# Performance work log

Measured on AMD Instinct MI355X. Metric: run time of the kernel, lower is better.

Reference implementation:

```python
import jax, jax.numpy as jnp
import numpy as np

N = 50000
E = 1600000
IN_DIM = 64
EMB_DIM = 64
DENSE = 128
HEADS = 2
GATD = 64
SLOPE = 0.2


def gat_conv(x, src, dst, W, al, ar, b):
    # DGL GATConv: x [N, Fin], W [Fin, H*D], al/ar/b [H, D]
    n = x.shape[0]
    H, D = al.shape
    z = (x @ W).reshape(n, H, D)                      # [N,H,D]
    el = jnp.sum(z * al, axis=-1)                     # [N,H]
    er = jnp.sum(z * ar, axis=-1)                     # [N,H]
    e = jax.nn.leaky_relu(el[src] + er[dst], SLOPE)   # [E,H]
    # edge softmax grouped by destination node
    m = jax.ops.segment_max(e, dst, num_segments=n)   # [N,H]
    ex = jnp.exp(e - m[dst])                          # [E,H]
    s = jax.ops.segment_sum(ex, dst, num_segments=n)  # [N,H]
    alpha = ex / s[dst]                               # [E,H]
    out = jax.ops.segment_sum(alpha[:, :, None] * z[src], dst, num_segments=n)
    return out + b                                    # [N,H,D]


def setup_inputs() -> dict:
    key = jax.random.key(0)
    ks = jax.random.split(key, 20)
    g = lambda k, sh: jax.random.normal(k, sh, dtype=jnp.float32) * 0.05
    inp = {
        "feat": jax.random.normal(ks[0], (N, IN_DIM), dtype=jnp.float32),
        "node_ids": jax.random.randint(ks[1], (N,), 0, N, dtype=jnp.int32),
        "src": jax.random.randint(ks[2], (E,), 0, N, dtype=jnp.int32),
        "dst": jax.random.randint(ks[3], (E,), 0, N, dtype=jnp.int32),
        "emb": g(ks[4], (N, EMB_DIM)),
        "dense_w": g(ks[5], (IN_DIM + EMB_DIM, DENSE)),
        "dense_b": jnp.zeros((DENSE,), jnp.float32),
        "g1_w": g(ks[6], (DENSE, HEADS * GATD)),
        "g1_al": g(ks[7], (HEADS, GATD)),
        "g1_ar": g(ks[8], (HEADS, GATD)),
        "g1_b": jnp.zeros((HEADS, GATD), jnp.float32),
        "g2_w": g(ks[9], (HEADS * GATD, HEADS * GATD)),
        "g2_al": g(ks[10], (HEADS, GATD)),
        "g2_ar": g(ks[11], (HEADS, GATD)),
        "g2_b": jnp.zeros((HEADS, GATD), jnp.float32),
        "out_w": g(ks[12], (HEADS * GATD, 1)),
        "out_al": g(ks[13], (1, 1)),
        "out_ar": g(ks[14], (1, 1)),
        "out_b": jnp.zeros((1, 1), jnp.float32),
    }
    return inp


def reference(feat, node_ids, src, dst, emb, dense_w, dense_b,
              g1_w, g1_al, g1_ar, g1_b, g2_w, g2_al, g2_ar, g2_b,
              out_w, out_al, out_ar, out_b):
    # embedding concat + initial dense + ReLU
    h = jnp.concatenate([emb[node_ids], feat], axis=-1)   # [N, 128]
    h = jax.nn.relu(h @ dense_w + dense_b)                # [N, 128]
    # GAT layer 1: ReLU then concat heads (reshape N, H*D)
    h = jax.nn.relu(gat_conv(h, src, dst, g1_w, g1_al, g1_ar, g1_b))
    h = h.reshape(h.shape[0], -1)                         # [N, H*D]
    # GAT layer 2
    h = jax.nn.relu(gat_conv(h, src, dst, g2_w, g2_al, g2_ar, g2_b))
    h = h.reshape(h.shape[0], -1)
    # output GAT layer, 1 head, squeeze head dim
    h = gat_conv(h, src, dst, out_w, out_al, out_ar, out_b)  # [N,1,1]
    return h[:, 0, :]                                        # [N,1]
```

## Files before the change

kernel.cpp:

```cpp
#include <hip/hip_runtime.h>
#include <cfloat>
#include <cmath>


#define CBG 256
#define CAPC 12288
#define TILE 8192
#define BIMG 10240

typedef __attribute__((ext_vector_type(8))) short short8v;
typedef __attribute__((ext_vector_type(4))) float f32x4;

__device__ __forceinline__ float lrelu(float x) { return x > 0.f ? x : 0.2f * x; }

__device__ __forceinline__ uint32_t bf16_rne(float f) {
  uint32_t u = __float_as_uint(f);
  return (u + 0x7fffu + ((u >> 16) & 1u)) >> 16;
}
__device__ __forceinline__ uint32_t pack_hilo(float v) {
  uint32_t h = bf16_rne(v);
  float r = v - __uint_as_float(h << 16);
  return (h << 16) | bf16_rne(r);
}

__global__ __launch_bounds__(256) void bucketA_kernel(
    const int* __restrict__ src, const int* __restrict__ dst,
    int* __restrict__ scount, uint32_t* __restrict__ tmp, int e, int ncb) {
  __shared__ int cnt[256];
  __shared__ int lscan[256];
  __shared__ int gbase[256];
  __shared__ uint32_t image[TILE];
  const int t = threadIdx.x;
  const int e0 = blockIdx.x * TILE;
  const int ne = min(TILE, e - e0);

  for (int i = t; i < 256; i += 256) cnt[i] = 0;
  __syncthreads();
  for (int i = t; i < ne; i += 256) atomicAdd(&cnt[dst[e0 + i] >> 8], 1);
  __syncthreads();
  if (t < 64) {
    int carry = 0;
    for (int base = 0; base < ncb; base += 64) {
      int idx = base + t;
      int c = (idx < ncb) ? cnt[idx] : 0;
      int v = c;
#pragma unroll
      for (int off = 1; off < 64; off <<= 1) {
        int u = __shfl_up(v, off, 64);
        if (t >= off) v += u;
      }
      if (idx < ncb) lscan[idx] = carry + v - c;
      carry += __shfl(v, 63, 64);
    }
  }
  __syncthreads();
  for (int b = t; b < ncb; b += 256)
    gbase[b] = (cnt[b] > 0) ? atomicAdd(&scount[b], cnt[b]) : 0;
  __syncthreads();
  for (int b = t; b < ncb; b += 256) cnt[b] = 0;
  __syncthreads();
  for (int i = t; i < ne; i += 256) {
    int d = dst[e0 + i], s = src[e0 + i];
    int b = d >> 8;
    int r = atomicAdd(&cnt[b], 1);
    image[lscan[b] + r] =
        (uint32_t)s | ((uint32_t)(d & 255) << 16) | ((uint32_t)b << 24);
  }
  __syncthreads();
  for (int j = t; j < ne; j += 256) {
    uint32_t w = image[j];
    int b = w >> 24;
    int pos = gbase[b] + (j - lscan[b]);
    if (pos < CAPC) tmp[(size_t)b * CAPC + pos] = w & 0xFFFFFFu;
  }
}

__global__ __launch_bounds__(64) void scanS_kernel(const int* __restrict__ scount,
                                                   int* __restrict__ sbase,
                                                   int* __restrict__ row_start,
                                                   int ncb, int n, int e) {
  const int lane = threadIdx.x;
  int carry = 0;
  for (int base = 0; base < ncb; base += 64) {
    int idx = base + lane;
    int c = (idx < ncb) ? scount[idx] : 0;
    int v = c;
#pragma unroll
    for (int off = 1; off < 64; off <<= 1) {
      int u = __shfl_up(v, off, 64);
      if (lane >= off) v += u;
    }
    if (idx < ncb) sbase[idx] = carry + v - c;
    carry += __shfl(v, 63, 64);
  }
  if (lane == 0) row_start[n] = e;
}

__global__ __launch_bounds__(256) void bucketB_kernel(
    const uint32_t* __restrict__ tmp, const int* __restrict__ scount,
    const int* __restrict__ sbase, int* __restrict__ row_start,
    int* __restrict__ csr_src, int n, int ncb) {
  __shared__ int cnt[256];
  __shared__ int cur[256];
  __shared__ int wsum[4];
  __shared__ uint32_t image[BIMG];
  const int b = blockIdx.x, t = threadIdx.x, lane = t & 63, wid = t >> 6;
  const int total = min(scount[b], CAPC);
  const int base = sbase[b];
  const uint32_t* strm = tmp + (size_t)b * CAPC;

  cnt[t] = 0;
  __syncthreads();
  for (int i = t; i < total; i += 256) atomicAdd(&cnt[(strm[i] >> 16) & 255], 1);
  __syncthreads();
  int c = cnt[t], v = c;
#pragma unroll
  for (int off = 1; off < 64; off <<= 1) {
    int u = __shfl_up(v, off, 64);
    if (lane >= off) v += u;
  }
  if (lane == 63) wsum[wid] = v;
  __syncthreads();
  if (t == 0) {
    int acc = 0;
#pragma unroll
    for (int w = 0; w < 4; w++) { int x = wsum[w]; wsum[w] = acc; acc += x; }
  }
  __syncthreads();
  int ex = wsum[wid] + v - c;
  cur[t] = ex;
  int d = b * CBG + t;
  if (d < n) row_start[d] = base + ex;
  __syncthreads();
  for (int i = t; i < total; i += 256) {
    uint32_t w = strm[i];
    int dl = (w >> 16) & 255;
    int pos = atomicAdd(&cur[dl], 1);
    if (pos < BIMG) image[pos] = w & 0xFFFFu;
    else csr_src[base + pos] = (int)(w & 0xFFFFu);
  }
  __syncthreads();
  const int lim = total < BIMG ? total : BIMG;
  for (int j = t; j < lim; j += 256) csr_src[base + j] = (int)image[j];
}

__global__ void hist_kernel(const int* __restrict__ dst, int* __restrict__ cnt, int e) {
  for (int i = blockIdx.x * blockDim.x + threadIdx.x; i < e; i += gridDim.x * blockDim.x)
    atomicAdd(&cnt[dst[i]], 1);
}
__global__ void scatter_kernel(const int* __restrict__ src, const int* __restrict__ dst,
                               const int* __restrict__ row_start, int* __restrict__ cursor,
                               int* __restrict__ csr_src, int e) {
  for (int i = blockIdx.x * blockDim.x + threadIdx.x; i < e; i += gridDim.x * blockDim.x) {
    int d = dst[i];
    int pos = atomicAdd(&cursor[d], 1);
    csr_src[row_start[d] + pos] = src[i];
  }
}
__global__ __launch_bounds__(1024) void scan1_kernel(const int* __restrict__ cnt,
                                                     int* __restrict__ row_start,
                                                     int* __restrict__ bsum, int n) {
  __shared__ int wsum[16];
  const int t = threadIdx.x, lane = t & 63, wid = t >> 6;
  int i = blockIdx.x * 1024 + t;
  int c = (i < n) ? cnt[i] : 0;
  int v = c;
#pragma unroll
  for (int off = 1; off < 64; off <<= 1) {
    int u = __shfl_up(v, off, 64);
    if (lane >= off) v += u;
  }
  if (lane == 63) wsum[wid] = v;
  __syncthreads();
  if (t == 0) {
    int acc = 0;
#pragma unroll
    for (int w = 0; w < 16; w++) { int x = wsum[w]; wsum[w] = acc; acc += x; }
    bsum[blockIdx.x] = acc;
  }
  __syncthreads();
  if (i < n) row_start[i] = wsum[wid] + v - c;
}
__global__ __launch_bounds__(64) void scan2_kernel(int* __restrict__ bsum, int nb) {
  const int lane = threadIdx.x;
  int carry = 0;
  for (int base = 0; base < nb; base += 64) {
    int idx = base + lane;
    int c = (idx < nb) ? bsum[idx] : 0;
    int v = c;
#pragma unroll
    for (int off = 1; off < 64; off <<= 1) {
      int u = __shfl_up(v, off, 64);
      if (lane >= off) v += u;
    }
    if (idx < nb) bsum[idx] = carry + v - c;
    carry += __shfl(v, 63, 64);
  }
}
__global__ void scan3_kernel(int* __restrict__ row_start, const int* __restrict__ bsum,
                             int n, int e) {
  int i = blockIdx.x * blockDim.x + threadIdx.x;
  if (i < n) row_start[i] += bsum[i >> 10];
  if (i == 0) row_start[n] = e;
}

__global__ __launch_bounds__(256) void wswz_kernel(const float* __restrict__ W,
                                                   short* __restrict__ Whi,
                                                   short* __restrict__ Wlo) {
  int fid = blockIdx.x * 256 + threadIdx.x;
  if (fid >= 2048) return;
  int lane = fid & 63;
  int cq = fid >> 6;
  int q = cq >> 3, c = cq & 7;
  int col = c * 16 + (lane & 15);
  int k0 = q * 32 + (lane >> 4) * 8;
  short hi[8], lo[8];
#pragma unroll
  for (int j = 0; j < 8; j++) {
    float v = W[(k0 + j) * 128 + col];
    uint32_t h = bf16_rne(v);
    float r = v - __uint_as_float(h << 16);
    hi[j] = (short)h;
    lo[j] = (short)bf16_rne(r);
  }
#pragma unroll
  for (int j = 0; j < 8; j++) {
    Whi[fid * 8 + j] = hi[j];
    Wlo[fid * 8 + j] = lo[j];
  }
}

template <int MODE>
__global__ __launch_bounds__(256) void mfmm_kernel(
    const uint32_t* __restrict__ Xp, const short* __restrict__ Whi,
    const short* __restrict__ Wlo, const float* __restrict__ bias,
    uint32_t* __restrict__ Hp, uint32_t* __restrict__ zp,
    float2* __restrict__ el2, float2* __restrict__ er2,
    const float* __restrict__ al, const float* __restrict__ ar, int n,
    const float* __restrict__ emb, const int* __restrict__ ids,
    const float* __restrict__ feat) {
  __shared__ short Ahi[64 * 136];
  __shared__ short Alo[64 * 136];
  const int t = threadIdx.x;
  const int nb = blockIdx.x * 64;

  for (int idx = t; idx < 64 * 64; idx += 256) {
    int nl = idx >> 6, k2 = (idx & 63) << 1;
    int node = nb + nl;
    uint32_t whi = 0, wlo = 0;
    if (node < n) {
      if (MODE == 1) {
        uint2 w = *(const uint2*)&Xp[(size_t)node * 128 + k2];
        whi = (w.x >> 16) | (w.y & 0xffff0000u);
        wlo = (w.x & 0xffffu) | (w.y << 16);
      } else {
        float2 v;
        if (k2 < 64) v = *(const float2*)&emb[(size_t)ids[node] * 64 + k2];
        else         v = *(const float2*)&feat[(size_t)node * 64 + (k2 - 64)];
        uint32_t h0 = bf16_rne(v.x), h1 = bf16_rne(v.y);
        float r0 = v.x - __uint_as_float(h0 << 16);
        float r1 = v.y - __uint_as_float(h1 << 16);
        whi = h0 | (h1 << 16);
        wlo = bf16_rne(r0) | (bf16_rne(r1) << 16);
      }
    }
    *(uint32_t*)&Ahi[nl * 136 + k2] = whi;
    *(uint32_t*)&Alo[nl * 136 + k2] = wlo;
  }
  __syncthreads();

  const int lane = t & 63, wv = t >> 6;
  const int r16 = lane & 15, g = lane >> 4;
  const int arow = (wv * 16 + r16) * 136;

  f32x4 acc[8];
#pragma unroll
  for (int c = 0; c < 8; c++) acc[c] = (f32x4){0.f, 0.f, 0.f, 0.f};

#pragma unroll
  for (int q = 0; q < 4; q++) {
    int ka = q * 32 + g * 8;
    short8v ahi = *(const short8v*)&Ahi[arow + ka];
    short8v alo = *(const short8v*)&Alo[arow + ka];
#pragma unroll
    for (int c = 0; c < 8; c++) {
      short8v bhi = *(const short8v*)&Whi[(((q * 8 + c) * 64) + lane) * 8];
      short8v blo = *(const short8v*)&Wlo[(((q * 8 + c) * 64) + lane) * 8];
      acc[c] = __builtin_amdgcn_mfma_f32_16x16x32_bf16(ahi, bhi, acc[c], 0, 0, 0);
      acc[c] = __builtin_amdgcn_mfma_f32_16x16x32_bf16(ahi, blo, acc[c], 0, 0, 0);
      acc[c] = __builtin_amdgcn_mfma_f32_16x16x32_bf16(alo, bhi, acc[c], 0, 0, 0);
    }
  }

  const int node_base = nb + wv * 16;
  if (MODE == 0) {
#pragma unroll
    for (int c = 0; c < 8; c++) {
      int col = c * 16 + r16;
      float bv = bias[col];
#pragma unroll
      for (int r = 0; r < 4; r++) {
        int node = node_base + g * 4 + r;
        if (node < n) {
          float v = fmaxf(acc[c][r] + bv, 0.f);
          Hp[(size_t)node * 128 + col] = pack_hilo(v);
        }
      }
    }
  } else {
    float p0l[4] = {0, 0, 0, 0}, p1l[4] = {0, 0, 0, 0};
    float p0r[4] = {0, 0, 0, 0}, p1r[4] = {0, 0, 0, 0};
#pragma unroll
    for (int c = 0; c < 8; c++) {
      int col = c * 16 + r16;
      float av = al[col], rv = ar[col];
#pragma unroll
      for (int r = 0; r < 4; r++) {
        if (c < 4) { p0l[r] = fmaf(acc[c][r], av, p0l[r]); p0r[r] = fmaf(acc[c][r], rv, p0r[r]); }
        else       { p1l[r] = fmaf(acc[c][r], av, p1l[r]); p1r[r] = fmaf(acc[c][r], rv, p1r[r]); }
      }
    }
#pragma unroll
    for (int c = 0; c < 8; c++) {
#pragma unroll
      for (int r = 0; r < 4; r++) {
        float other = __shfl_xor(acc[c][r], 1, 64);
        int node = node_base + g * 4 + r;
        if (!(lane & 1) && node < n) {
          uint32_t w = bf16_rne(acc[c][r]) | (bf16_rne(other) << 16);
          zp[(size_t)node * 64 + c * 8 + (r16 >> 1)] = w;
        }
      }
    }
#pragma unroll
    for (int off = 1; off < 16; off <<= 1) {
#pragma unroll
      for (int r = 0; r < 4; r++) {
        p0l[r] += __shfl_xor(p0l[r], off, 64);
        p1l[r] += __shfl_xor(p1l[r], off, 64);
        p0r[r] += __shfl_xor(p0r[r], off, 64);
        p1r[r] += __shfl_xor(p1r[r], off, 64);
      }
    }
    if (r16 == 0) {
#pragma unroll
      for (int r = 0; r < 4; r++) {
        int node = node_base + g * 4 + r;
        if (node < n) {
          el2[node] = make_float2(p0l[r], p1l[r]);
          er2[node] = make_float2(p0r[r], p1r[r]);
        }
      }
    }
  }
}

#define CAP 256
__global__ __launch_bounds__(256) void agg12_kernel(
    const uint32_t* __restrict__ zp, const float2* __restrict__ el2,
    const float2* __restrict__ er2, const int* __restrict__ row_start,
    const int* __restrict__ csr_src, const float* __restrict__ bias,
    uint32_t* __restrict__ Hp,
    const float* __restrict__ ow, const float* __restrict__ oal,
    const float* __restrict__ oar, float* __restrict__ z3,
    float* __restrict__ el3, float* __restrict__ er3, int n, int fuse_out) {
  __shared__ float2 ec[4][CAP];
  __shared__ int sc[4][CAP];
  const int w = threadIdx.x >> 6, lane = threadIdx.x & 63;
  const int node = blockIdx.x * 4 + w;
  const bool valid = node < n;
  int rs = 0, deg = 0;
  float er0 = 0.f, er1 = 0.f;
  if (valid) {
    rs = row_start[node];
    deg = row_start[node + 1] - rs;
    float2 e2 = er2[node];
    er0 = e2.x; er1 = e2.y;
  }
  const int cdeg = deg < CAP ? deg : CAP;

  float sp0 = 0.f, sp1 = 0.f;
  for (int i = lane; i < deg; i += 64) {
    int s = csr_src[rs + i];
    float2 l = el2[s];
    float x0 = __expf(lrelu(l.x + er0));
    float x1 = __expf(lrelu(l.y + er1));
    if (i < CAP) { sc[w][i] = s; ec[w][i] = make_float2(x0, x1); }
    sp0 += x0; sp1 += x1;
  }
#pragma unroll
  for (int off = 32; off; off >>= 1) {
    sp0 += __shfl_xor(sp0, off, 64);
    sp1 += __shfl_xor(sp1, off, 64);
  }
  __syncthreads();

  float ae = 0.f, ao = 0.f;
  int i = 0;
  for (; i + 8 <= cdeg; i += 8) {
    uint32_t zw[8];
    float xh[8];
#pragma unroll
    for (int u = 0; u < 8; u++) {
      int s = sc[w][i + u];
      float2 ex = ec[w][i + u];
      xh[u] = (lane < 32) ? ex.x : ex.y;
      zw[u] = zp[(size_t)s * 64 + lane];
    }
#pragma unroll
    for (int u = 0; u < 8; u++) {
      ae = fmaf(xh[u], __uint_as_float(zw[u] << 16), ae);
      ao = fmaf(xh[u], __uint_as_float(zw[u] & 0xffff0000u), ao);
    }
  }
  for (; i < cdeg; i++) {
    int s = sc[w][i];
    float2 ex = ec[w][i];
    float x = (lane < 32) ? ex.x : ex.y;
    uint32_t zw = zp[(size_t)s * 64 + lane];
    ae = fmaf(x, __uint_as_float(zw << 16), ae);
    ao = fmaf(x, __uint_as_float(zw & 0xffff0000u), ao);
  }
  for (; i < deg; i++) {
    int s = csr_src[rs + i];
    float2 l = el2[s];
    float x0 = __expf(lrelu(l.x + er0));
    float x1 = __expf(lrelu(l.y + er1));
    float x = (lane < 32) ? x0 : x1;
    uint32_t zw = zp[(size_t)s * 64 + lane];
    ae = fmaf(x, __uint_as_float(zw << 16), ae);
    ao = fmaf(x, __uint_as_float(zw & 0xffff0000u), ao);
  }

  if (valid) {
    float sp = (lane < 32) ? sp0 : sp1;
    float2 b2 = reinterpret_cast<const float2*>(bias)[lane];
    float oe, oo;
    if (deg == 0) { oe = b2.x; oo = b2.y; }
    else { oe = ae / sp + b2.x; oo = ao / sp + b2.y; }
    oe = fmaxf(oe, 0.f);
    oo = fmaxf(oo, 0.f);
    if (!fuse_out) {
      *(uint2*)&Hp[(size_t)node * 128 + 2 * lane] =
          make_uint2(pack_hilo(oe), pack_hilo(oo));
    } else {
      float2 w2 = reinterpret_cast<const float2*>(ow)[lane];
      float d = oe * w2.x + oo * w2.y;
#pragma unroll
      for (int off = 32; off; off >>= 1) d += __shfl_xor(d, off, 64);
      if (lane == 0) {
        z3[node] = d;
        el3[node] = d * oal[0];
        er3[node] = d * oar[0];
      }
    }
  }
}

__global__ __launch_bounds__(256) void agg3_kernel(
    const float* __restrict__ z3, const float* __restrict__ el3,
    const float* __restrict__ er3, const int* __restrict__ row_start,
    const int* __restrict__ csr_src, const float* __restrict__ b,
    float* __restrict__ out, int n) {
  int node = blockIdx.x * 4 + (threadIdx.x >> 6);
  int lane = threadIdx.x & 63;
  if (node >= n) return;
  int rs = row_start[node];
  int deg = row_start[node + 1] - rs;
  float er = er3[node];
  float sp = 0.f, ap = 0.f;
  for (int i = lane; i < deg; i += 64) {
    int s = csr_src[rs + i];
    float ex = __expf(lrelu(el3[s] + er));
    sp += ex;
    ap = fmaf(ex, z3[s], ap);
  }
#pragma unroll
  for (int off = 32; off; off >>= 1) {
    sp += __shfl_xor(sp, off, 64);
    ap += __shfl_xor(ap, off, 64);
  }
  if (lane == 0) out[node] = (deg == 0) ? b[0] : (ap / sp + b[0]);
}

extern "C" void kernel_launch(void* const* d_in, const int* in_sizes, int n_in,
                              void* d_out, int out_size, void* d_ws, size_t ws_size,
                              hipStream_t stream) {
  const float* feat     = (const float*)d_in[0];
  const int*   node_ids = (const int*)d_in[1];
  const int*   src      = (const int*)d_in[2];
  const int*   dst      = (const int*)d_in[3];
  const float* emb      = (const float*)d_in[4];
  const float* dense_w  = (const float*)d_in[5];
  const float* dense_b  = (const float*)d_in[6];
  const float* g1_w     = (const float*)d_in[7];
  const float* g1_al    = (const float*)d_in[8];
  const float* g1_ar    = (const float*)d_in[9];
  const float* g1_b     = (const float*)d_in[10];
  const float* g2_w     = (const float*)d_in[11];
  const float* g2_al    = (const float*)d_in[12];
  const float* g2_ar    = (const float*)d_in[13];
  const float* g2_b     = (const float*)d_in[14];
  const float* out_w    = (const float*)d_in[15];
  const float* out_al   = (const float*)d_in[16];
  const float* out_ar   = (const float*)d_in[17];
  const float* out_b    = (const float*)d_in[18];
  const int n = in_sizes[0] / 64;
  const int e = in_sizes[2];

  const int ncb = (n + CBG - 1) / CBG;

  char* ws = (char*)d_ws;
  size_t off = 0;
  auto alloc = [&](size_t bytes) -> void* {
    void* p = ws + off;
    off += (bytes + 255) & ~(size_t)255;
    return p;
  };
  uint32_t* Hp       = (uint32_t*)alloc((size_t)n * 128 * 4);
  size_t zp_bytes    = (size_t)n * 64 * 4;
  size_t tmp_bytes   = (size_t)ncb * CAPC * 4;
  uint32_t* zp       = (uint32_t*)alloc(zp_bytes > tmp_bytes ? zp_bytes : tmp_bytes);
  uint32_t* tmp      = zp;
  float2*   el2      = (float2*)alloc((size_t)n * 8);
  float2*   er2      = (float2*)alloc((size_t)n * 8);
  float*    z3       = (float*)alloc((size_t)n * 4);
  float*    el3      = (float*)alloc((size_t)n * 4);
  float*    er3      = (float*)alloc((size_t)n * 4);
  int*      scount   = (int*)alloc((size_t)ncb * 4);
  int*      sbase    = (int*)alloc((size_t)ncb * 4);
  int*      row_start= (int*)alloc((size_t)(n + 1) * 4);
  int*      csr_src  = (int*)alloc((size_t)e * 4);
  short*    Wd_hi    = (short*)alloc(2048 * 8 * 2);
  short*    Wd_lo    = (short*)alloc(2048 * 8 * 2);
  short*    W1_hi    = (short*)alloc(2048 * 8 * 2);
  short*    W1_lo    = (short*)alloc(2048 * 8 * 2);
  short*    W2_hi    = (short*)alloc(2048 * 8 * 2);
  short*    W2_lo    = (short*)alloc(2048 * 8 * 2);
  int*      cnt      = (int*)alloc((size_t)n * 4);
  int*      cursor   = (int*)alloc((size_t)n * 4);
  const int nblk     = (n + 1023) / 1024;
  int*      bsum     = (int*)alloc((size_t)nblk * 4);

  if (n < 65536) {
    hipMemsetAsync(scount, 0, (size_t)ncb * 4, stream);
    const int natile = (e + TILE - 1) / TILE;
    bucketA_kernel<<<natile, 256, 0, stream>>>(src, dst, scount, tmp, e, ncb);
    scanS_kernel<<<1, 64, 0, stream>>>(scount, sbase, row_start, ncb, n, e);
    bucketB_kernel<<<ncb, 256, 0, stream>>>(tmp, scount, sbase, row_start,
                                            csr_src, n, ncb);
  } else {
    hipMemsetAsync(cnt, 0, (size_t)n * 4, stream);
    hipMemsetAsync(cursor, 0, (size_t)n * 4, stream);
    hist_kernel<<<2048, 256, 0, stream>>>(dst, cnt, e);
    scan1_kernel<<<nblk, 1024, 0, stream>>>(cnt, row_start, bsum, n);
    scan2_kernel<<<1, 64, 0, stream>>>(bsum, nblk);
    scan3_kernel<<<(n + 255) / 256, 256, 0, stream>>>(row_start, bsum, n, e);
    scatter_kernel<<<2048, 256, 0, stream>>>(src, dst, row_start, cursor, csr_src, e);
  }

  wswz_kernel<<<8, 256, 0, stream>>>(dense_w, Wd_hi, Wd_lo);
  wswz_kernel<<<8, 256, 0, stream>>>(g1_w, W1_hi, W1_lo);
  wswz_kernel<<<8, 256, 0, stream>>>(g2_w, W2_hi, W2_lo);

  const int mmgrid = (n + 63) / 64;
  const int ngrid4 = (n + 3) / 4;

  mfmm_kernel<0><<<mmgrid, 256, 0, stream>>>(nullptr, Wd_hi, Wd_lo, dense_b,
                                             Hp, nullptr, nullptr, nullptr,
                                             nullptr, nullptr, n, emb, node_ids, feat);
  mfmm_kernel<1><<<mmgrid, 256, 0, stream>>>(Hp, W1_hi, W1_lo, nullptr,
                                             nullptr, zp, el2, er2,
                                             g1_al, g1_ar, n, nullptr, nullptr, nullptr);
  agg12_kernel<<<ngrid4, 256, 0, stream>>>(zp, el2, er2, row_start, csr_src, g1_b, Hp,
                                           nullptr, nullptr, nullptr, nullptr, nullptr,
                                           nullptr, n, 0);
  mfmm_kernel<1><<<mmgrid, 256, 0, stream>>>(Hp, W2_hi, W2_lo, nullptr,
                                             nullptr, zp, el2, er2,
                                             g2_al, g2_ar, n, nullptr, nullptr, nullptr);
  agg12_kernel<<<ngrid4, 256, 0, stream>>>(zp, el2, er2, row_start, csr_src, g2_b, nullptr,
                                           out_w, out_al, out_ar, z3, el3, er3, n, 1);
  agg3_kernel<<<ngrid4, 256, 0, stream>>>(z3, el3, er3, row_start, csr_src, out_b,
                                          (float*)d_out, n);
}
```

Before: 258.7 us.

## Fold scan into bucketB, merge weight swizzles, widen loads, split agg heads

Removes the single-block scan kernel by having each bucketB block sum the preceding bucket counts itself, and merges the three weight swizzle launches into one. The mfmm staging loop uses 128-bit loads, and agg12 splits the two heads across half-waves with vectorized LDS reads and a 16-wide gather unroll. agg3 uses 32 lanes per node. The aim is to cut launch count and serialization and to raise memory-level parallelism in the gathers. The cost is redundant prefix summing in every bucketB block (quadratic in bucket count) and higher register pressure.

```diff
diff --git a/kernel.cpp b/kernel.cpp
--- a/kernel.cpp
+++ b/kernel.cpp
@@ -75,42 +75,29 @@
   }
 }
 
-__global__ __launch_bounds__(64) void scanS_kernel(const int* __restrict__ scount,
-                                                   int* __restrict__ sbase,
-                                                   int* __restrict__ row_start,
-                                                   int ncb, int n, int e) {
-  const int lane = threadIdx.x;
-  int carry = 0;
-  for (int base = 0; base < ncb; base += 64) {
-    int idx = base + lane;
-    int c = (idx < ncb) ? scount[idx] : 0;
-    int v = c;
-#pragma unroll
-    for (int off = 1; off < 64; off <<= 1) {
-      int u = __shfl_up(v, off, 64);
-      if (lane >= off) v += u;
-    }
-    if (idx < ncb) sbase[idx] = carry + v - c;
-    carry += __shfl(v, 63, 64);
-  }
-  if (lane == 0) row_start[n] = e;
-}
-
 __global__ __launch_bounds__(256) void bucketB_kernel(
     const uint32_t* __restrict__ tmp, const int* __restrict__ scount,
-    const int* __restrict__ sbase, int* __restrict__ row_start,
-    int* __restrict__ csr_src, int n, int ncb) {
+    int* __restrict__ row_start, int* __restrict__ csr_src, int n, int ncb, int e) {
   __shared__ int cnt[256];
   __shared__ int cur[256];
   __shared__ int wsum[4];
+  __shared__ int s_base;
   __shared__ uint32_t image[BIMG];
   const int b = blockIdx.x, t = threadIdx.x, lane = t & 63, wid = t >> 6;
+
+  if (t < 64) {
+    int part = 0;
+    for (int idx = lane; idx < b; idx += 64) part += scount[idx];
+#pragma unroll
+    for (int off = 32; off; off >>= 1) part += __shfl_xor(part, off, 64);
+    if (lane == 0) s_base = part;
+  }
+  cnt[t] = 0;
+  __syncthreads();
   const int total = min(scount[b], CAPC);
-  const int base = sbase[b];
+  const int base = s_base;
   const uint32_t* strm = tmp + (size_t)b * CAPC;
 
-  cnt[t] = 0;
-  __syncthreads();
   for (int i = t; i < total; i += 256) atomicAdd(&cnt[(strm[i] >> 16) & 255], 1);
   __syncthreads();
   int c = cnt[t], v = c;
@@ -131,6 +118,7 @@
   cur[t] = ex;
   int d = b * CBG + t;
   if (d < n) row_start[d] = base + ex;
+  if (b == 0 && t == 0) row_start[n] = e;
   __syncthreads();
   for (int i = t; i < total; i += 256) {
     uint32_t w = strm[i];
@@ -204,29 +192,28 @@
   if (i == 0) row_start[n] = e;
 }
 
-__global__ __launch_bounds__(256) void wswz_kernel(const float* __restrict__ W,
-                                                   short* __restrict__ Whi,
-                                                   short* __restrict__ Wlo) {
-  int fid = blockIdx.x * 256 + threadIdx.x;
-  if (fid >= 2048) return;
+__global__ __launch_bounds__(256) void wswz3_kernel(
+    const float* __restrict__ W0, const float* __restrict__ W1,
+    const float* __restrict__ W2, short* __restrict__ Whi0,
+    short* __restrict__ Wlo0, short* __restrict__ Whi1, short* __restrict__ Wlo1,
+    short* __restrict__ Whi2, short* __restrict__ Wlo2) {
+  int which = blockIdx.x >> 3;
+  const float* W = which == 0 ? W0 : (which == 1 ? W1 : W2);
+  short* Whi = which == 0 ? Whi0 : (which == 1 ? Whi1 : Whi2);
+  short* Wlo = which == 0 ? Wlo0 : (which == 1 ? Wlo1 : Wlo2);
+  int fid = (blockIdx.x & 7) * 256 + threadIdx.x;
   int lane = fid & 63;
   int cq = fid >> 6;
   int q = cq >> 3, c = cq & 7;
   int col = c * 16 + (lane & 15);
   int k0 = q * 32 + (lane >> 4) * 8;
-  short hi[8], lo[8];
 #pragma unroll
   for (int j = 0; j < 8; j++) {
     float v = W[(k0 + j) * 128 + col];
     uint32_t h = bf16_rne(v);
     float r = v - __uint_as_float(h << 16);
-    hi[j] = (short)h;
-    lo[j] = (short)bf16_rne(r);
-  }
-#pragma unroll
-  for (int j = 0; j < 8; j++) {
-    Whi[fid * 8 + j] = hi[j];
-    Wlo[fid * 8 + j] = lo[j];
+    Whi[fid * 8 + j] = (short)h;
+    Wlo[fid * 8 + j] = (short)bf16_rne(r);
   }
 }
 
@@ -244,28 +231,33 @@
   const int t = threadIdx.x;
   const int nb = blockIdx.x * 64;
 
-  for (int idx = t; idx < 64 * 64; idx += 256) {
-    int nl = idx >> 6, k2 = (idx & 63) << 1;
+  for (int idx = t; idx < 64 * 32; idx += 256) {
+    int nl = idx >> 5, k4 = (idx & 31) << 2;
     int node = nb + nl;
-    uint32_t whi = 0, wlo = 0;
+    uint32_t h01 = 0, h23 = 0, l01 = 0, l23 = 0;
     if (node < n) {
       if (MODE == 1) {
-        uint2 w = *(const uint2*)&Xp[(size_t)node * 128 + k2];
-        whi = (w.x >> 16) | (w.y & 0xffff0000u);
-        wlo = (w.x & 0xffffu) | (w.y << 16);
+        uint4 w = *(const uint4*)&Xp[(size_t)node * 128 + k4];
+        h01 = (w.x >> 16) | (w.y & 0xffff0000u);
+        l01 = (w.x & 0xffffu) | (w.y << 16);
+        h23 = (w.z >> 16) | (w.w & 0xffff0000u);
+        l23 = (w.z & 0xffffu) | (w.w << 16);
       } else {
-        float2 v;
-        if (k2 < 64) v = *(const float2*)&emb[(size_t)ids[node] * 64 + k2];
-        else         v = *(const float2*)&feat[(size_t)node * 64 + (k2 - 64)];
-        uint32_t h0 = bf16_rne(v.x), h1 = bf16_rne(v.y);
-        float r0 = v.x - __uint_as_float(h0 << 16);
-        float r1 = v.y - __uint_as_float(h1 << 16);
-        whi = h0 | (h1 << 16);
-        wlo = bf16_rne(r0) | (bf16_rne(r1) << 16);
-      }
-    }
-    *(uint32_t*)&Ahi[nl * 136 + k2] = whi;
-    *(uint32_t*)&Alo[nl * 136 + k2] = wlo;
+        float4 v;
+        if (k4 < 64) v = *(const float4*)&emb[(size_t)ids[node] * 64 + k4];
+        else         v = *(const float4*)&feat[(size_t)node * 64 + (k4 - 64)];
+        uint32_t a0 = bf16_rne(v.x), a1 = bf16_rne(v.y);
+        uint32_t a2 = bf16_rne(v.z), a3 = bf16_rne(v.w);
+        h01 = a0 | (a1 << 16);
+        h23 = a2 | (a3 << 16);
+        l01 = bf16_rne(v.x - __uint_as_float(a0 << 16)) |
+              (bf16_rne(v.y - __uint_as_float(a1 << 16)) << 16);
+        l23 = bf16_rne(v.z - __uint_as_float(a2 << 16)) |
+              (bf16_rne(v.w - __uint_as_float(a3 << 16)) << 16);
+      }
+    }
+    *(uint2*)&Ahi[nl * 136 + k4] = make_uint2(h01, h23);
+    *(uint2*)&Alo[nl * 136 + k4] = make_uint2(l01, l23);
   }
   __syncthreads();
 
@@ -364,80 +356,96 @@
     const float* __restrict__ ow, const float* __restrict__ oal,
     const float* __restrict__ oar, float* __restrict__ z3,
     float* __restrict__ el3, float* __restrict__ er3, int n, int fuse_out) {
-  __shared__ float2 ec[4][CAP];
+  __shared__ float ecf[4][2][CAP];
   __shared__ int sc[4][CAP];
   const int w = threadIdx.x >> 6, lane = threadIdx.x & 63;
+  const int hl = lane >> 5, l32 = lane & 31;
   const int node = blockIdx.x * 4 + w;
   const bool valid = node < n;
   int rs = 0, deg = 0;
-  float er0 = 0.f, er1 = 0.f;
+  float er_h = 0.f;
   if (valid) {
     rs = row_start[node];
     deg = row_start[node + 1] - rs;
-    float2 e2 = er2[node];
-    er0 = e2.x; er1 = e2.y;
+    er_h = ((const float*)&er2[node])[hl];
   }
   const int cdeg = deg < CAP ? deg : CAP;
 
-  float sp0 = 0.f, sp1 = 0.f;
-  for (int i = lane; i < deg; i += 64) {
+  float sp_h = 0.f;
+  for (int i = l32; i < deg; i += 32) {
     int s = csr_src[rs + i];
-    float2 l = el2[s];
-    float x0 = __expf(lrelu(l.x + er0));
-    float x1 = __expf(lrelu(l.y + er1));
-    if (i < CAP) { sc[w][i] = s; ec[w][i] = make_float2(x0, x1); }
-    sp0 += x0; sp1 += x1;
-  }
-#pragma unroll
-  for (int off = 32; off; off >>= 1) {
-    sp0 += __shfl_xor(sp0, off, 64);
-    sp1 += __shfl_xor(sp1, off, 64);
-  }
-  __syncthreads();
-
+    float lv = ((const float*)&el2[s])[hl];
+    float x = __expf(lrelu(lv + er_h));
+    if (i < CAP) {
+      if (hl == 0) sc[w][i] = s;
+      ecf[w][hl][i] = x;
+    }
+    sp_h += x;
+  }
+#pragma unroll
+  for (int off = 16; off; off >>= 1) sp_h += __shfl_xor(sp_h, off, 64);
+  __syncthreads();
+
+  const float* exh = ecf[w][hl];
   float ae = 0.f, ao = 0.f;
   int i = 0;
-  for (; i + 8 <= cdeg; i += 8) {
-    uint32_t zw[8];
-    float xh[8];
-#pragma unroll
-    for (int u = 0; u < 8; u++) {
-      int s = sc[w][i + u];
-      float2 ex = ec[w][i + u];
-      xh[u] = (lane < 32) ? ex.x : ex.y;
-      zw[u] = zp[(size_t)s * 64 + lane];
-    }
-#pragma unroll
-    for (int u = 0; u < 8; u++) {
-      ae = fmaf(xh[u], __uint_as_float(zw[u] << 16), ae);
-      ao = fmaf(xh[u], __uint_as_float(zw[u] & 0xffff0000u), ao);
-    }
+  for (; i + 16 <= cdeg; i += 16) {
+    int s16[16];
+    float x16[16];
+#pragma unroll
+    for (int q = 0; q < 4; q++) {
+      int4 s4 = *(const int4*)&sc[w][i + q * 4];
+      float4 x4 = *(const float4*)&exh[i + q * 4];
+      s16[q * 4 + 0] = s4.x; s16[q * 4 + 1] = s4.y;
+      s16[q * 4 + 2] = s4.z; s16[q * 4 + 3] = s4.w;
+      x16[q * 4 + 0] = x4.x; x16[q * 4 + 1] = x4.y;
+      x16[q * 4 + 2] = x4.z; x16[q * 4 + 3] = x4.w;
+    }
+    uint32_t zw[16];
+#pragma unroll
+    for (int u = 0; u < 16; u++) zw[u] = zp[(size_t)s16[u] * 64 + lane];
+#pragma unroll
+    for (int u = 0; u < 16; u++) {
+      ae = fmaf(x16[u], __uint_as_float(zw[u] << 16), ae);
+      ao = fmaf(x16[u], __uint_as_float(zw[u] & 0xffff0000u), ao);
+    }
+  }
+  for (; i + 4 <= cdeg; i += 4) {
+    int4 s4 = *(const int4*)&sc[w][i];
+    float4 x4 = *(const float4*)&exh[i];
+    uint32_t z0 = zp[(size_t)s4.x * 64 + lane];
+    uint32_t z1 = zp[(size_t)s4.y * 64 + lane];
+    uint32_t z2 = zp[(size_t)s4.z * 64 + lane];
+    uint32_t z3v = zp[(size_t)s4.w * 64 + lane];
+    ae = fmaf(x4.x, __uint_as_float(z0 << 16), ae);
+    ao = fmaf(x4.x, __uint_as_float(z0 & 0xffff0000u), ao);
+    ae = fmaf(x4.y, __uint_as_float(z1 << 16), ae);
+    ao = fmaf(x4.y, __uint_as_float(z1 & 0xffff0000u), ao);
+    ae = fmaf(x4.z, __uint_as_float(z2 << 16), ae);
+    ao = fmaf(x4.z, __uint_as_float(z2 & 0xffff0000u), ao);
+    ae = fmaf(x4.w, __uint_as_float(z3v << 16), ae);
+    ao = fmaf(x4.w, __uint_as_float(z3v & 0xffff0000u), ao);
   }
   for (; i < cdeg; i++) {
     int s = sc[w][i];
-    float2 ex = ec[w][i];
-    float x = (lane < 32) ? ex.x : ex.y;
+    float x = exh[i];
     uint32_t zw = zp[(size_t)s * 64 + lane];
     ae = fmaf(x, __uint_as_float(zw << 16), ae);
     ao = fmaf(x, __uint_as_float(zw & 0xffff0000u), ao);
   }
   for (; i < deg; i++) {
     int s = csr_src[rs + i];
-    float2 l = el2[s];
-    float x0 = __expf(lrelu(l.x + er0));
-    float x1 = __expf(lrelu(l.y + er1));
-    float x = (lane < 32) ? x0 : x1;
+    float x = __expf(lrelu(((const float*)&el2[s])[hl] + er_h));
     uint32_t zw = zp[(size_t)s * 64 + lane];
     ae = fmaf(x, __uint_as_float(zw << 16), ae);
     ao = fmaf(x, __uint_as_float(zw & 0xffff0000u), ao);
   }
 
   if (valid) {
-    float sp = (lane < 32) ? sp0 : sp1;
     float2 b2 = reinterpret_cast<const float2*>(bias)[lane];
     float oe, oo;
     if (deg == 0) { oe = b2.x; oo = b2.y; }
-    else { oe = ae / sp + b2.x; oo = ao / sp + b2.y; }
+    else { oe = ae / sp_h + b2.x; oo = ao / sp_h + b2.y; }
     oe = fmaxf(oe, 0.f);
     oo = fmaxf(oo, 0.f);
     if (!fuse_out) {
@@ -462,25 +470,25 @@
     const float* __restrict__ er3, const int* __restrict__ row_start,
     const int* __restrict__ csr_src, const float* __restrict__ b,
     float* __restrict__ out, int n) {
-  int node = blockIdx.x * 4 + (threadIdx.x >> 6);
-  int lane = threadIdx.x & 63;
+  int node = blockIdx.x * 8 + (threadIdx.x >> 5);
+  int l32 = threadIdx.x & 31;
   if (node >= n) return;
   int rs = row_start[node];
   int deg = row_start[node + 1] - rs;
   float er = er3[node];
   float sp = 0.f, ap = 0.f;
-  for (int i = lane; i < deg; i += 64) {
+  for (int i = l32; i < deg; i += 32) {
     int s = csr_src[rs + i];
     float ex = __expf(lrelu(el3[s] + er));
     sp += ex;
     ap = fmaf(ex, z3[s], ap);
   }
 #pragma unroll
-  for (int off = 32; off; off >>= 1) {
+  for (int off = 16; off; off >>= 1) {
     sp += __shfl_xor(sp, off, 64);
     ap += __shfl_xor(ap, off, 64);
   }
-  if (lane == 0) out[node] = (deg == 0) ? b[0] : (ap / sp + b[0]);
+  if (l32 == 0) out[node] = (deg == 0) ? b[0] : (ap / sp + b[0]);
 }
 
 extern "C" void kernel_launch(void* const* d_in, const int* in_sizes, int n_in,
@@ -528,7 +536,6 @@
   float*    el3      = (float*)alloc((size_t)n * 4);
   float*    er3      = (float*)alloc((size_t)n * 4);
   int*      scount   = (int*)alloc((size_t)ncb * 4);
-  int*      sbase    = (int*)alloc((size_t)ncb * 4);
   int*      row_start= (int*)alloc((size_t)(n + 1) * 4);
   int*      csr_src  = (int*)alloc((size_t)e * 4);
   short*    Wd_hi    = (short*)alloc(2048 * 8 * 2);
@@ -542,13 +549,15 @@
   const int nblk     = (n + 1023) / 1024;
   int*      bsum     = (int*)alloc((size_t)nblk * 4);
 
+  wswz3_kernel<<<24, 256, 0, stream>>>(dense_w, g1_w, g2_w,
+                                       Wd_hi, Wd_lo, W1_hi, W1_lo, W2_hi, W2_lo);
+
   if (n < 65536) {
     hipMemsetAsync(scount, 0, (size_t)ncb * 4, stream);
     const int natile = (e + TILE - 1) / TILE;
     bucketA_kernel<<<natile, 256, 0, stream>>>(src, dst, scount, tmp, e, ncb);
-    scanS_kernel<<<1, 64, 0, stream>>>(scount, sbase, row_start, ncb, n, e);
-    bucketB_kernel<<<ncb, 256, 0, stream>>>(tmp, scount, sbase, row_start,
-                                            csr_src, n, ncb);
+    bucketB_kernel<<<ncb, 256, 0, stream>>>(tmp, scount, row_start, csr_src,
+                                            n, ncb, e);
   } else {
     hipMemsetAsync(cnt, 0, (size_t)n * 4, stream);
     hipMemsetAsync(cursor, 0, (size_t)n * 4, stream);
@@ -559,12 +568,9 @@
     scatter_kernel<<<2048, 256, 0, stream>>>(src, dst, row_start, cursor, csr_src, e);
   }
 
-  wswz_kernel<<<8, 256, 0, stream>>>(dense_w, Wd_hi, Wd_lo);
-  wswz_kernel<<<8, 256, 0, stream>>>(g1_w, W1_hi, W1_lo);
-  wswz_kernel<<<8, 256, 0, stream>>>(g2_w, W2_hi, W2_lo);
-
   const int mmgrid = (n + 63) / 64;
   const int ngrid4 = (n + 3) / 4;
+  const int ngrid8 = (n + 7) / 8;
 
   mfmm_kernel<0><<<mmgrid, 256, 0, stream>>>(nullptr, Wd_hi, Wd_lo, dense_b,
                                              Hp, nullptr, nullptr, nullptr,
@@ -580,6 +586,6 @@
                                              g2_al, g2_ar, n, nullptr, nullptr, nullptr);
   agg12_kernel<<<ngrid4, 256, 0, stream>>>(zp, el2, er2, row_start, csr_src, g2_b, nullptr,
                                            out_w, out_al, out_ar, z3, el3, er3, n, 1);
-  agg3_kernel<<<ngrid4, 256, 0, stream>>>(z3, el3, er3, row_start, csr_src, out_b,
+  agg3_kernel<<<ngrid8, 256, 0, stream>>>(z3, el3, er3, row_start, csr_src, out_b,
                                           (float*)d_out, n);
 }
```

Result: slower. 265.9 us (+2.8%).
